# Kernel tuning notes

Measured on AMD Instinct MI355X. Metric: run time of the kernel, lower is better.

## Reference

```python
import jax, jax.numpy as jnp
import numpy as np


def setup_inputs() -> dict:
    key = jax.random.key(0)
    k1, = jax.random.split(key, 1)
    B, H, W, C = 16, 64, 64, 256
    x = jax.random.normal(k1, (B, H, W, C), dtype=jnp.float32)
    gamma = jnp.zeros((1,), dtype=jnp.float32)
    return {"x": x, "gamma": gamma}


def reference(x, gamma):
    B, H, W, C = x.shape
    a = x.reshape(B, H * W, C)                      # [B, HW, C]
    # aTa[b, i, j] = sum_n a[b, n, i] * a[b, n, j]  -> [B, C, C]
    aTa = jnp.einsum('bni,bnj->bij', a, a)
    attn = jax.nn.softmax(aTa, axis=-1)             # softmax over last channel axis
    # aaTa[b, n, j] = sum_i a[b, n, i] * attn[b, i, j]
    aaTa = jnp.einsum('bni,bij->bnj', a, attn)      # [B, HW, C]
    aaTa = aaTa.reshape(B, H, W, C)
    return gamma * aaTa + x
```

## Files before the change

### kernel.cpp

```cpp
#include <hip/hip_runtime.h>
#include <hip/hip_bf16.h>


#define BB 16
#define NN 4096
#define CC 256
#define SPLITK 8
#define KCHUNK (NN / SPLITK)

typedef __attribute__((ext_vector_type(4))) short short4v;
typedef __attribute__((ext_vector_type(8))) short short8v;
typedef __attribute__((ext_vector_type(4))) float floatx4;

__device__ __forceinline__ unsigned short f2bf(float f) {
    unsigned int u = __float_as_uint(f);
    u += 0x7fffu + ((u >> 16) & 1u);
    return (unsigned short)(u >> 16);
}
__device__ __forceinline__ short4v cvt4(floatx4 v) {
    short4v r;
    r[0] = (short)f2bf(v[0]); r[1] = (short)f2bf(v[1]);
    r[2] = (short)f2bf(v[2]); r[3] = (short)f2bf(v[3]);
    return r;
}

__global__ __launch_bounds__(256) void k_transpose(const float* __restrict__ x,
                                                   unsigned short* __restrict__ aT) {
    __shared__ unsigned short tile[64 * 68];
    const int b  = blockIdx.z;
    const int n0 = blockIdx.x * 64;
    const int c0 = blockIdx.y * 64;
    const int t  = threadIdx.x;
    const int q4 = (t & 15) * 4;
    const int tr = t >> 4;

    const float* xb = x + ((size_t)b * NN + n0) * CC + c0;
    for (int r = 0; r < 4; ++r) {
        int row = tr + 16 * r;
        floatx4 v = *(const floatx4*)(xb + (size_t)row * CC + q4);
        *(short4v*)&tile[row * 68 + q4] = cvt4(v);
    }
    __syncthreads();
    unsigned short* aTb = aT + ((size_t)b * CC + c0) * NN + n0;
    for (int r = 0; r < 4; ++r) {
        int c = tr + 16 * r;
        short4v v;
        v[0] = (short)tile[(q4 + 0) * 68 + c];
        v[1] = (short)tile[(q4 + 1) * 68 + c];
        v[2] = (short)tile[(q4 + 2) * 68 + c];
        v[3] = (short)tile[(q4 + 3) * 68 + c];
        *(short4v*)(aTb + (size_t)c * NN + q4) = v;
    }
}

__global__ __launch_bounds__(256) void k_gemm1(const unsigned short* __restrict__ aT,
                                               float* __restrict__ part) {
    __shared__ unsigned short Ap[64 * 72];
    __shared__ unsigned short Bp[256 * 72];
    const int i0    = blockIdx.x * 64;
    const int b     = blockIdx.y;
    const int split = blockIdx.z;
    const int t  = threadIdx.x;
    const int w  = t >> 6, l = t & 63;
    const int lk = (l >> 4) * 8;
    const int lm = l & 15;
    const int sc = t >> 4;
    const int sk = (t & 15) * 4;

    const unsigned short* Abase = aT + ((size_t)b * CC + i0) * NN;
    const unsigned short* Bbase = aT + (size_t)b * CC * NN;

    floatx4 acc[4][4] = {};
    const int kbeg = split * KCHUNK;
    for (int k0 = kbeg; k0 < kbeg + KCHUNK; k0 += 64) {
        #pragma unroll
        for (int r = 0; r < 4; ++r) {
            int i = sc + 16 * r;
            *(short4v*)&Ap[i * 72 + sk] = *(const short4v*)(Abase + (size_t)i * NN + k0 + sk);
        }
        #pragma unroll
        for (int r = 0; r < 16; ++r) {
            int j = sc + 16 * r;
            *(short4v*)&Bp[j * 72 + sk] = *(const short4v*)(Bbase + (size_t)j * NN + k0 + sk);
        }
        __syncthreads();
        #pragma unroll
        for (int ks = 0; ks < 64; ks += 32) {
            short8v af[4], bf[4];
            #pragma unroll
            for (int mt = 0; mt < 4; ++mt)
                af[mt] = *(const short8v*)&Ap[(mt * 16 + lm) * 72 + ks + lk];
            #pragma unroll
            for (int nt = 0; nt < 4; ++nt)
                bf[nt] = *(const short8v*)&Bp[(w * 64 + nt * 16 + lm) * 72 + ks + lk];
            #pragma unroll
            for (int mt = 0; mt < 4; ++mt)
                #pragma unroll
                for (int nt = 0; nt < 4; ++nt)
                    acc[mt][nt] = __builtin_amdgcn_mfma_f32_16x16x32_bf16(af[mt], bf[nt], acc[mt][nt], 0, 0, 0);
        }
        __syncthreads();
    }
    const int orow = (l >> 4) * 4;
    float* pout = part + ((size_t)(split * BB + b) * CC) * CC;
    #pragma unroll
    for (int mt = 0; mt < 4; ++mt)
        #pragma unroll
        for (int nt = 0; nt < 4; ++nt)
            #pragma unroll
            for (int r = 0; r < 4; ++r) {
                int i = i0 + mt * 16 + orow + r;
                int j = w * 64 + nt * 16 + lm;
                pout[(size_t)i * CC + j] = acc[mt][nt][r];
            }
}

__global__ __launch_bounds__(256) void k_softmax(const float* __restrict__ part,
                                                 unsigned short* __restrict__ attnT) {
    const int w = threadIdx.x >> 6;
    const int l = threadIdx.x & 63;
    const int row = blockIdx.x * 4 + w;
    const int b = row >> 8;
    const int i = row & 255;
    float v0 = 0.f, v1 = 0.f, v2 = 0.f, v3 = 0.f;
    #pragma unroll
    for (int s = 0; s < SPLITK; ++s) {
        const float* p = part + ((size_t)(s * BB + b) * CC + i) * CC;
        v0 += p[l]; v1 += p[l + 64]; v2 += p[l + 128]; v3 += p[l + 192];
    }
    float m = fmaxf(fmaxf(v0, v1), fmaxf(v2, v3));
    for (int off = 32; off >= 1; off >>= 1) m = fmaxf(m, __shfl_xor(m, off, 64));
    v0 = __expf(v0 - m); v1 = __expf(v1 - m); v2 = __expf(v2 - m); v3 = __expf(v3 - m);
    float s = v0 + v1 + v2 + v3;
    for (int off = 32; off >= 1; off >>= 1) s += __shfl_xor(s, off, 64);
    float rs = 1.0f / s;
    unsigned short* o = attnT + (size_t)b * CC * CC + i;
    o[(size_t)(l +   0) * CC] = f2bf(v0 * rs);
    o[(size_t)(l +  64) * CC] = f2bf(v1 * rs);
    o[(size_t)(l + 128) * CC] = f2bf(v2 * rs);
    o[(size_t)(l + 192) * CC] = f2bf(v3 * rs);
}

__global__ __launch_bounds__(256) void k_gemm2(const float* __restrict__ x,
                                               const unsigned short* __restrict__ attnT,
                                               const float* __restrict__ gamma,
                                               float* __restrict__ out) {
    __shared__ unsigned short At[64 * 72];
    __shared__ unsigned short Bt[256 * 72];
    const int n0 = blockIdx.x * 64;
    const int b  = blockIdx.y;
    const int t  = threadIdx.x;
    const int w  = t >> 6, l = t & 63;
    const int lk = (l >> 4) * 8, lm = l & 15;
    const int sc = t >> 4, sk = (t & 15) * 4;

    const float*          Abase = x + ((size_t)b * NN + n0) * CC;
    const unsigned short* Bbase = attnT + (size_t)b * CC * CC;

    floatx4 acc[4][4] = {};
    for (int k0 = 0; k0 < CC; k0 += 64) {
        #pragma unroll
        for (int r = 0; r < 4; ++r) {
            int n = sc + 16 * r;
            floatx4 av = *(const floatx4*)(Abase + (size_t)n * CC + k0 + sk);
            *(short4v*)&At[n * 72 + sk] = cvt4(av);
        }
        #pragma unroll
        for (int r = 0; r < 16; ++r) {
            int j = sc + 16 * r;
            *(short4v*)&Bt[j * 72 + sk] = *(const short4v*)(Bbase + (size_t)j * CC + k0 + sk);
        }
        __syncthreads();
        #pragma unroll
        for (int ks = 0; ks < 64; ks += 32) {
            short8v af[4], bf[4];
            #pragma unroll
            for (int mt = 0; mt < 4; ++mt)
                af[mt] = *(const short8v*)&At[(mt * 16 + lm) * 72 + ks + lk];
            #pragma unroll
            for (int nt = 0; nt < 4; ++nt)
                bf[nt] = *(const short8v*)&Bt[(w * 64 + nt * 16 + lm) * 72 + ks + lk];
            #pragma unroll
            for (int mt = 0; mt < 4; ++mt)
                #pragma unroll
                for (int nt = 0; nt < 4; ++nt)
                    acc[mt][nt] = __builtin_amdgcn_mfma_f32_16x16x32_bf16(af[mt], bf[nt], acc[mt][nt], 0, 0, 0);
        }
        __syncthreads();
    }
    const float g = gamma[0];
    const int orow = (l >> 4) * 4;
    #pragma unroll
    for (int mt = 0; mt < 4; ++mt)
        #pragma unroll
        for (int nt = 0; nt < 4; ++nt)
            #pragma unroll
            for (int r = 0; r < 4; ++r) {
                int nr = n0 + mt * 16 + orow + r;
                int j  = w * 64 + nt * 16 + lm;
                size_t idx = ((size_t)b * NN + nr) * CC + j;
                out[idx] = g * acc[mt][nt][r] + x[idx];
            }
}

extern "C" void kernel_launch(void* const* d_in, const int* in_sizes, int n_in,
                              void* d_out, int out_size, void* d_ws, size_t ws_size,
                              hipStream_t stream) {
    const float* x     = (const float*)d_in[0];
    const float* gamma = (const float*)d_in[1];
    float* out = (float*)d_out;

    char* ws = (char*)d_ws;
    unsigned short* aT    = (unsigned short*)ws;
    float*          part  = (float*)(ws + (size_t)BB * CC * NN * 2);
    unsigned short* attnT = (unsigned short*)(ws + (size_t)BB * CC * NN * 2
                                                 + (size_t)SPLITK * BB * CC * CC * 4);

    k_transpose<<<dim3(NN / 64, CC / 64, BB), 256, 0, stream>>>(x, aT);
    k_gemm1   <<<dim3(CC / 64, BB, SPLITK),   256, 0, stream>>>(aT, part);
    k_softmax <<<dim3(BB * CC / 4),           256, 0, stream>>>(part, attnT);
    k_gemm2   <<<dim3(NN / 64, BB),           256, 0, stream>>>(x, attnT, gamma, out);
}
```

Baseline: 180.3 us.

## Load MFMA fragments directly from global and precompute bf16 copy of x

Both GEMM kernels stop staging tiles through shared memory and barriers, and instead read MFMA operand fragments straight from global memory into registers, relying on cache for reuse. The prep kernel now also writes a row-major bf16 copy of x, so the second GEMM reads half the bytes and skips the per-tile fp32-to-bf16 conversion. The residual add now uses the bf16-rounded x instead of the fp32 input, which loses precision in the output. The direct global loads also risk poorer coalescing and more cache traffic in place of LDS reuse.

```diff
diff --git a/kernel.cpp b/kernel.cpp
--- a/kernel.cpp
+++ b/kernel.cpp
@@ -17,6 +17,9 @@
     u += 0x7fffu + ((u >> 16) & 1u);
     return (unsigned short)(u >> 16);
 }
+__device__ __forceinline__ float bf2f(unsigned short u) {
+    return __uint_as_float(((unsigned int)u) << 16);
+}
 __device__ __forceinline__ short4v cvt4(floatx4 v) {
     short4v r;
     r[0] = (short)f2bf(v[0]); r[1] = (short)f2bf(v[1]);
@@ -24,8 +27,9 @@
     return r;
 }
 
-__global__ __launch_bounds__(256) void k_transpose(const float* __restrict__ x,
-                                                   unsigned short* __restrict__ aT) {
+__global__ __launch_bounds__(256) void k_prep(const float* __restrict__ x,
+                                              unsigned short* __restrict__ aT,
+                                              unsigned short* __restrict__ xbf) {
     __shared__ unsigned short tile[64 * 68];
     const int b  = blockIdx.z;
     const int n0 = blockIdx.x * 64;
@@ -35,10 +39,13 @@
     const int tr = t >> 4;
 
     const float* xb = x + ((size_t)b * NN + n0) * CC + c0;
+    unsigned short* xbfb = xbf + ((size_t)b * NN + n0) * CC + c0;
     for (int r = 0; r < 4; ++r) {
         int row = tr + 16 * r;
         floatx4 v = *(const floatx4*)(xb + (size_t)row * CC + q4);
-        *(short4v*)&tile[row * 68 + q4] = cvt4(v);
+        short4v s = cvt4(v);
+        *(short4v*)&tile[row * 68 + q4] = s;
+        *(short4v*)(xbfb + (size_t)row * CC + q4) = s;
     }
     __syncthreads();
     unsigned short* aTb = aT + ((size_t)b * CC + c0) * NN + n0;
@@ -55,8 +62,6 @@
 
 __global__ __launch_bounds__(256) void k_gemm1(const unsigned short* __restrict__ aT,
                                                float* __restrict__ part) {
-    __shared__ unsigned short Ap[64 * 72];
-    __shared__ unsigned short Bp[256 * 72];
     const int i0    = blockIdx.x * 64;
     const int b     = blockIdx.y;
     const int split = blockIdx.z;
@@ -64,42 +69,30 @@
     const int w  = t >> 6, l = t & 63;
     const int lk = (l >> 4) * 8;
     const int lm = l & 15;
-    const int sc = t >> 4;
-    const int sk = (t & 15) * 4;
-
-    const unsigned short* Abase = aT + ((size_t)b * CC + i0) * NN;
-    const unsigned short* Bbase = aT + (size_t)b * CC * NN;
+
+    const unsigned short* arow[4];
+    const unsigned short* brow[4];
+    #pragma unroll
+    for (int mt = 0; mt < 4; ++mt)
+        arow[mt] = aT + ((size_t)b * CC + i0 + mt * 16 + lm) * NN + lk;
+    #pragma unroll
+    for (int nt = 0; nt < 4; ++nt)
+        brow[nt] = aT + ((size_t)b * CC + w * 64 + nt * 16 + lm) * NN + lk;
 
     floatx4 acc[4][4] = {};
     const int kbeg = split * KCHUNK;
-    for (int k0 = kbeg; k0 < kbeg + KCHUNK; k0 += 64) {
-        #pragma unroll
-        for (int r = 0; r < 4; ++r) {
-            int i = sc + 16 * r;
-            *(short4v*)&Ap[i * 72 + sk] = *(const short4v*)(Abase + (size_t)i * NN + k0 + sk);
-        }
-        #pragma unroll
-        for (int r = 0; r < 16; ++r) {
-            int j = sc + 16 * r;
-            *(short4v*)&Bp[j * 72 + sk] = *(const short4v*)(Bbase + (size_t)j * NN + k0 + sk);
-        }
-        __syncthreads();
-        #pragma unroll
-        for (int ks = 0; ks < 64; ks += 32) {
-            short8v af[4], bf[4];
-            #pragma unroll
-            for (int mt = 0; mt < 4; ++mt)
-                af[mt] = *(const short8v*)&Ap[(mt * 16 + lm) * 72 + ks + lk];
+    #pragma unroll 4
+    for (int k0 = kbeg; k0 < kbeg + KCHUNK; k0 += 32) {
+        short8v af[4], bf[4];
+        #pragma unroll
+        for (int mt = 0; mt < 4; ++mt) af[mt] = *(const short8v*)(arow[mt] + k0);
+        #pragma unroll
+        for (int nt = 0; nt < 4; ++nt) bf[nt] = *(const short8v*)(brow[nt] + k0);
+        #pragma unroll
+        for (int mt = 0; mt < 4; ++mt)
             #pragma unroll
             for (int nt = 0; nt < 4; ++nt)
-                bf[nt] = *(const short8v*)&Bp[(w * 64 + nt * 16 + lm) * 72 + ks + lk];
-            #pragma unroll
-            for (int mt = 0; mt < 4; ++mt)
-                #pragma unroll
-                for (int nt = 0; nt < 4; ++nt)
-                    acc[mt][nt] = __builtin_amdgcn_mfma_f32_16x16x32_bf16(af[mt], bf[nt], acc[mt][nt], 0, 0, 0);
-        }
-        __syncthreads();
+                acc[mt][nt] = __builtin_amdgcn_mfma_f32_16x16x32_bf16(af[mt], bf[nt], acc[mt][nt], 0, 0, 0);
     }
     const int orow = (l >> 4) * 4;
     float* pout = part + ((size_t)(split * BB + b) * CC) * CC;
@@ -141,52 +134,38 @@
     o[(size_t)(l + 192) * CC] = f2bf(v3 * rs);
 }
 
-__global__ __launch_bounds__(256) void k_gemm2(const float* __restrict__ x,
-                                               const unsigned short* __restrict__ attnT,
-                                               const float* __restrict__ gamma,
-                                               float* __restrict__ out) {
-    __shared__ unsigned short At[64 * 72];
-    __shared__ unsigned short Bt[256 * 72];
+__global__ __launch_bounds__(256, 4) void k_gemm2(const unsigned short* __restrict__ xbf,
+                                                  const unsigned short* __restrict__ attnT,
+                                                  const float* __restrict__ gamma,
+                                                  float* __restrict__ out) {
     const int n0 = blockIdx.x * 64;
     const int b  = blockIdx.y;
     const int t  = threadIdx.x;
     const int w  = t >> 6, l = t & 63;
     const int lk = (l >> 4) * 8, lm = l & 15;
-    const int sc = t >> 4, sk = (t & 15) * 4;
-
-    const float*          Abase = x + ((size_t)b * NN + n0) * CC;
-    const unsigned short* Bbase = attnT + (size_t)b * CC * CC;
+
+    const unsigned short* arow[4];
+    const unsigned short* brow[4];
+    #pragma unroll
+    for (int mt = 0; mt < 4; ++mt)
+        arow[mt] = xbf + ((size_t)b * NN + n0 + mt * 16 + lm) * CC + lk;
+    #pragma unroll
+    for (int nt = 0; nt < 4; ++nt)
+        brow[nt] = attnT + ((size_t)b * CC + w * 64 + nt * 16 + lm) * CC + lk;
 
     floatx4 acc[4][4] = {};
-    for (int k0 = 0; k0 < CC; k0 += 64) {
-        #pragma unroll
-        for (int r = 0; r < 4; ++r) {
-            int n = sc + 16 * r;
-            floatx4 av = *(const floatx4*)(Abase + (size_t)n * CC + k0 + sk);
-            *(short4v*)&At[n * 72 + sk] = cvt4(av);
-        }
-        #pragma unroll
-        for (int r = 0; r < 16; ++r) {
-            int j = sc + 16 * r;
-            *(short4v*)&Bt[j * 72 + sk] = *(const short4v*)(Bbase + (size_t)j * CC + k0 + sk);
-        }
-        __syncthreads();
-        #pragma unroll
-        for (int ks = 0; ks < 64; ks += 32) {
-            short8v af[4], bf[4];
-            #pragma unroll
-            for (int mt = 0; mt < 4; ++mt)
-                af[mt] = *(const short8v*)&At[(mt * 16 + lm) * 72 + ks + lk];
+    #pragma unroll
+    for (int k0 = 0; k0 < CC; k0 += 32) {
+        short8v af[4], bf[4];
+        #pragma unroll
+        for (int mt = 0; mt < 4; ++mt) af[mt] = *(const short8v*)(arow[mt] + k0);
+        #pragma unroll
+        for (int nt = 0; nt < 4; ++nt) bf[nt] = *(const short8v*)(brow[nt] + k0);
+        #pragma unroll
+        for (int mt = 0; mt < 4; ++mt)
             #pragma unroll
             for (int nt = 0; nt < 4; ++nt)
-                bf[nt] = *(const short8v*)&Bt[(w * 64 + nt * 16 + lm) * 72 + ks + lk];
-            #pragma unroll
-            for (int mt = 0; mt < 4; ++mt)
-                #pragma unroll
-                for (int nt = 0; nt < 4; ++nt)
-                    acc[mt][nt] = __builtin_amdgcn_mfma_f32_16x16x32_bf16(af[mt], bf[nt], acc[mt][nt], 0, 0, 0);
-        }
-        __syncthreads();
+                acc[mt][nt] = __builtin_amdgcn_mfma_f32_16x16x32_bf16(af[mt], bf[nt], acc[mt][nt], 0, 0, 0);
     }
     const float g = gamma[0];
     const int orow = (l >> 4) * 4;
@@ -199,7 +178,7 @@
                 int nr = n0 + mt * 16 + orow + r;
                 int j  = w * 64 + nt * 16 + lm;
                 size_t idx = ((size_t)b * NN + nr) * CC + j;
-                out[idx] = g * acc[mt][nt][r] + x[idx];
+                out[idx] = g * acc[mt][nt][r] + bf2f(xbf[idx]);
             }
 }
 
@@ -212,12 +191,12 @@
 
     char* ws = (char*)d_ws;
     unsigned short* aT    = (unsigned short*)ws;
-    float*          part  = (float*)(ws + (size_t)BB * CC * NN * 2);
-    unsigned short* attnT = (unsigned short*)(ws + (size_t)BB * CC * NN * 2
-                                                 + (size_t)SPLITK * BB * CC * CC * 4);
-
-    k_transpose<<<dim3(NN / 64, CC / 64, BB), 256, 0, stream>>>(x, aT);
-    k_gemm1   <<<dim3(CC / 64, BB, SPLITK),   256, 0, stream>>>(aT, part);
-    k_softmax <<<dim3(BB * CC / 4),           256, 0, stream>>>(part, attnT);
-    k_gemm2   <<<dim3(NN / 64, BB),           256, 0, stream>>>(x, attnT, gamma, out);
-}
+    unsigned short* xbf   = (unsigned short*)(ws + (size_t)32 * 1024 * 1024);
+    float*          part  = (float*)(ws + (size_t)64 * 1024 * 1024);
+    unsigned short* attnT = (unsigned short*)(ws + (size_t)96 * 1024 * 1024);
+
+    k_prep   <<<dim3(NN / 64, CC / 64, BB), 256, 0, stream>>>(x, aT, xbf);
+    k_gemm1  <<<dim3(CC / 64, BB, SPLITK),  256, 0, stream>>>(aT, part);
+    k_softmax<<<dim3(BB * CC / 4),          256, 0, stream>>>(part, attnT);
+    k_gemm2  <<<dim3(NN / 64, BB),          256, 0, stream>>>(xbf, attnT, gamma, out);
+}
```

Measured after the change: 221.5 us. 1.23x slower.
